# Performance work log

Measured on AMD Instinct MI355X. Metric: run time of the kernel, lower is better.

Reference implementation:

```python
import jax, jax.numpy as jnp
import numpy as np

N_NODES = 100000
N_EDGES = 1600000
F_IN = 128
H = 128
N_GRAPHS = 64
NEG_SLOPE = 0.2  # PyG GATConv default


def setup_inputs() -> dict:
    key = jax.random.key(0)
    ks = jax.random.split(key, 9)
    x = jax.random.normal(ks[0], (N_NODES, F_IN), dtype=jnp.float32)
    edge_index = jax.random.randint(ks[1], (2, N_EDGES), 0, N_NODES, dtype=jnp.int32)
    batch = jnp.sort(jax.random.randint(ks[2], (N_NODES,), 0, N_GRAPHS, dtype=jnp.int32))
    W = jax.random.normal(ks[3], (F_IN, H), dtype=jnp.float32) * 0.05
    att_src = jax.random.normal(ks[4], (H,), dtype=jnp.float32) * 0.05
    att_dst = jax.random.normal(ks[5], (H,), dtype=jnp.float32) * 0.05
    bias = jax.random.normal(ks[6], (H,), dtype=jnp.float32) * 0.05
    fin_w = jax.random.normal(ks[7], (H, 1), dtype=jnp.float32) * 0.05
    fin_b = jax.random.normal(ks[8], (1,), dtype=jnp.float32) * 0.05
    return {"x": x, "edge_index": edge_index, "batch": batch, "W": W,
            "att_src": att_src, "att_dst": att_dst, "bias": bias,
            "fin_w": fin_w, "fin_b": fin_b}


def reference(x, edge_index, batch, W, att_src, att_dst, bias, fin_w, fin_b):
    n = x.shape[0]
    # add self loops (add_self_loops=True)
    loop = jnp.arange(n, dtype=edge_index.dtype)
    src = jnp.concatenate([edge_index[0], loop])  # [E+N]
    dst = jnp.concatenate([edge_index[1], loop])  # [E+N]
    h = x @ W                                     # [N,H]
    a_s = h @ att_src                             # [N]
    a_d = h @ att_dst                             # [N]
    e = jax.nn.leaky_relu(a_s[src] + a_d[dst], NEG_SLOPE)  # [E+N]
    # segment softmax over destination neighborhoods
    e_max = jax.ops.segment_max(e, dst, num_segments=n)
    e_exp = jnp.exp(e - e_max[dst])
    denom = jax.ops.segment_sum(e_exp, dst, num_segments=n)
    alpha = e_exp / denom[dst]                    # [E+N]
    agg = jax.ops.segment_sum(alpha[:, None] * h[src], dst, num_segments=n)  # [N,H]
    gnn_out = jax.nn.silu(agg + bias)             # [N,H]
    # global mean pool per graph
    cnt = jax.ops.segment_sum(jnp.ones((n,), dtype=x.dtype), batch, num_segments=N_GRAPHS)
    pooled = jax.ops.segment_sum(gnn_out, batch, num_segments=N_GRAPHS)
    pooled = pooled / jnp.maximum(cnt, 1.0)[:, None]  # [B,H]
    return pooled @ fin_w + fin_b                 # [B,1]
```

## Files before the change

### kernel.cpp

```cpp
#include <hip/hip_runtime.h>

#define NND 100000
#define NE  1600000
#define ET  (NE + NND)
#define HD  128
#define NGR 64
#define NEG 0.2f

#define PEB   16384
#define PBLK  ((ET + PEB - 1) / PEB)
#define NBK   ((NND + 511) / 512)

__device__ __forceinline__ unsigned f2bf(float x) {
  unsigned u = __builtin_bit_cast(unsigned, x);
  return (u + 0x7fffu + ((u >> 16) & 1u)) >> 16;
}
__device__ __forceinline__ float bflo(unsigned u) { return __builtin_bit_cast(float, u << 16); }
__device__ __forceinline__ float bfhi(unsigned u) { return __builtin_bit_cast(float, u & 0xffff0000u); }

__global__ __launch_bounds__(512, 1) void k_gemm(const float* __restrict__ x,
                                                 const float* __restrict__ W,
                                                 const float* __restrict__ att_s,
                                                 const float* __restrict__ att_d,
                                                 unsigned* __restrict__ h_bf,
                                                 float* __restrict__ a_s,
                                                 float* __restrict__ a_d) {
  __shared__ float Wl[128 * 128];
  __shared__ float xT[128 * 128];
  const int t = threadIdx.x;
  const int rbase = blockIdx.x * 128;
#pragma unroll
  for (int i = 0; i < 8; ++i) {
    int idx = i * 512 + t;
    int k = idx >> 5, j = (idx & 31) * 4;
    *(float4*)&Wl[k * 128 + j] = *(const float4*)&W[k * 128 + j];
  }
#pragma unroll
  for (int i = 0; i < 8; ++i) {
    int idx = i * 512 + t;
    int rl = idx >> 5, kq = idx & 31;
    int r = rbase + rl;
    float4 v = (r < NND) ? *(const float4*)&x[(size_t)r * 128 + kq * 4]
                         : make_float4(0.f, 0.f, 0.f, 0.f);
    int col = rl ^ ((kq & 7) << 2);
    xT[(kq * 4 + 0) * 128 + col] = v.x;
    xT[(kq * 4 + 1) * 128 + col] = v.y;
    xT[(kq * 4 + 2) * 128 + col] = v.z;
    xT[(kq * 4 + 3) * 128 + col] = v.w;
  }
  __syncthreads();
  const int tc = t & 15, tr = t >> 4;
  float acc[4][8] = {};
#pragma unroll 4
  for (int k = 0; k < 128; ++k) {
    int ra = (4 * tr) ^ (((k >> 2) & 7) << 2);
    float4 xa = *(const float4*)&xT[k * 128 + ra];
    float4 wa = *(const float4*)&Wl[k * 128 + 4 * tc];
    float4 wb = *(const float4*)&Wl[k * 128 + 64 + 4 * tc];
    float xr[4] = {xa.x, xa.y, xa.z, xa.w};
    float wc[8] = {wa.x, wa.y, wa.z, wa.w, wb.x, wb.y, wb.z, wb.w};
#pragma unroll
    for (int i = 0; i < 4; ++i)
#pragma unroll
      for (int j = 0; j < 8; ++j) acc[i][j] = fmaf(xr[i], wc[j], acc[i][j]);
  }
  float asv[8], adv[8];
  {
    float4 a0 = *(const float4*)&att_s[4 * tc];
    float4 a1 = *(const float4*)&att_s[64 + 4 * tc];
    asv[0]=a0.x; asv[1]=a0.y; asv[2]=a0.z; asv[3]=a0.w;
    asv[4]=a1.x; asv[5]=a1.y; asv[6]=a1.z; asv[7]=a1.w;
    float4 b0 = *(const float4*)&att_d[4 * tc];
    float4 b1 = *(const float4*)&att_d[64 + 4 * tc];
    adv[0]=b0.x; adv[1]=b0.y; adv[2]=b0.z; adv[3]=b0.w;
    adv[4]=b1.x; adv[5]=b1.y; adv[6]=b1.z; adv[7]=b1.w;
  }
#pragma unroll
  for (int i = 0; i < 4; ++i) {
    int r = rbase + 4 * tr + i;
    float ps = 0.f, pd = 0.f;
#pragma unroll
    for (int j = 0; j < 8; ++j) {
      ps = fmaf(acc[i][j], asv[j], ps);
      pd = fmaf(acc[i][j], adv[j], pd);
    }
#pragma unroll
    for (int o = 1; o < 16; o <<= 1) {
      ps += __shfl_xor(ps, o);
      pd += __shfl_xor(pd, o);
    }
    if (r < NND) {
      if (tc == 0) { a_s[r] = ps; a_d[r] = pd; }
      unsigned p0 = f2bf(acc[i][0]) | (f2bf(acc[i][1]) << 16);
      unsigned p1 = f2bf(acc[i][2]) | (f2bf(acc[i][3]) << 16);
      unsigned p2 = f2bf(acc[i][4]) | (f2bf(acc[i][5]) << 16);
      unsigned p3 = f2bf(acc[i][6]) | (f2bf(acc[i][7]) << 16);
      *(uint2*)&h_bf[(size_t)r * 64 + 2 * tc] = make_uint2(p0, p1);
      *(uint2*)&h_bf[(size_t)r * 64 + 32 + 2 * tc] = make_uint2(p2, p3);
    }
  }
}

__global__ __launch_bounds__(1024) void k_hist(const int* __restrict__ ei,
                                               int* __restrict__ hist) {
  __shared__ int hcnt[256];
  const int t = threadIdx.x;
  if (t < 256) hcnt[t] = 0;
  __syncthreads();
  const int base = blockIdx.x * PEB;
#pragma unroll
  for (int i = 0; i < PEB / 1024; ++i) {
    int e = base + i * 1024 + t;
    if (e < ET) {
      int d = (e < NE) ? ei[NE + e] : (e - NE);
      atomicAdd(&hcnt[d >> 9], 1);
    }
  }
  __syncthreads();
  if (t < 256) hist[blockIdx.x * 256 + t] = hcnt[t];
}

__global__ __launch_bounds__(256) void k_hoff(int* __restrict__ hist,
                                              int* __restrict__ bkoff,
                                              int* __restrict__ bkcnt) {
  __shared__ int sm[2][256];
  const int t = threadIdx.x;
  int run = 0;
  for (int b = 0; b < PBLK; ++b) {
    int v = hist[b * 256 + t];
    hist[b * 256 + t] = run;
    run += v;
  }
  sm[0][t] = run;
  __syncthreads();
  int c = 0;
  for (int o = 1; o < 256; o <<= 1) {
    int val = sm[c][t];
    if (t >= o) val += sm[c][t - o];
    sm[c ^ 1][t] = val;
    c ^= 1;
    __syncthreads();
  }
  int bstart = sm[c][t] - run;
  bkoff[t] = bstart;
  bkcnt[t] = run;
  for (int b = 0; b < PBLK; ++b) hist[b * 256 + t] += bstart;
}

__global__ __launch_bounds__(1024) void k_part(const int* __restrict__ ei,
                                               const int* __restrict__ hist,
                                               uint2* __restrict__ part) {
  __shared__ int hcur[256];
  const int t = threadIdx.x;
  if (t < 256) hcur[t] = hist[blockIdx.x * 256 + t];
  __syncthreads();
  const int base = blockIdx.x * PEB;
#pragma unroll
  for (int i = 0; i < PEB / 1024; ++i) {
    int e = base + i * 1024 + t;
    if (e < ET) {
      int s, d;
      if (e < NE) { s = ei[e]; d = ei[NE + e]; } else { s = e - NE; d = s; }
      int pos = atomicAdd(&hcur[d >> 9], 1);
      part[pos] = make_uint2((unsigned)s, (unsigned)d);
    }
  }
}

__global__ __launch_bounds__(256) void k_bdeg(const uint2* __restrict__ part,
                                              const int* __restrict__ bkoff,
                                              const int* __restrict__ bkcnt,
                                              int* __restrict__ deg) {
  __shared__ int dcnt[512];
  const int t = threadIdx.x;
  const int b = blockIdx.x;
  dcnt[t] = 0; dcnt[t + 256] = 0;
  __syncthreads();
  const int lo = bkoff[b], n = bkcnt[b];
  for (int i = t; i < n; i += 256)
    atomicAdd(&dcnt[part[lo + i].y & 511], 1);
  __syncthreads();
#pragma unroll
  for (int j = t; j < 512; j += 256) {
    int node = b * 512 + j;
    if (node < NND) deg[node] = dcnt[j];
  }
}

__global__ __launch_bounds__(256) void k_scan1(const int* __restrict__ deg,
                                               int* __restrict__ off,
                                               int* __restrict__ bsum) {
  __shared__ int sm[2][256];
  int t = threadIdx.x;
  int i = blockIdx.x * 256 + t;
  int v = (i < NND) ? deg[i] : 0;
  sm[0][t] = v;
  __syncthreads();
  int c = 0;
  for (int o = 1; o < 256; o <<= 1) {
    int val = sm[c][t];
    if (t >= o) val += sm[c][t - o];
    sm[c ^ 1][t] = val;
    c ^= 1;
    __syncthreads();
  }
  int incl = sm[c][t];
  if (i < NND) off[i] = incl - v;
  if (t == 255) bsum[blockIdx.x] = incl;
}

__global__ __launch_bounds__(512) void k_scan2(int* __restrict__ bsum) {
  __shared__ int sm[2][512];
  const int NB = 391;
  int t = threadIdx.x;
  int v = (t < NB) ? bsum[t] : 0;
  sm[0][t] = v;
  __syncthreads();
  int c = 0;
  for (int o = 1; o < 512; o <<= 1) {
    int val = sm[c][t];
    if (t >= o) val += sm[c][t - o];
    sm[c ^ 1][t] = val;
    c ^= 1;
    __syncthreads();
  }
  if (t < NB) bsum[t] = sm[c][t] - v;
}

__global__ void k_scan3(const int* __restrict__ bsum, int* __restrict__ off) {
  int i = blockIdx.x * 256 + threadIdx.x;
  if (i < NND) off[i] += bsum[blockIdx.x];
}

__global__ __launch_bounds__(256) void k_bscat(const uint2* __restrict__ part,
                                               const int* __restrict__ bkoff,
                                               const int* __restrict__ bkcnt,
                                               const int* __restrict__ off,
                                               int* __restrict__ esrc) {
  __shared__ int curl[512];
  const int t = threadIdx.x;
  const int b = blockIdx.x;
#pragma unroll
  for (int j = t; j < 512; j += 256) {
    int node = b * 512 + j;
    curl[j] = (node < NND) ? off[node] : 0;
  }
  __syncthreads();
  const int lo = bkoff[b], n = bkcnt[b];
  for (int i = t; i < n; i += 256) {
    uint2 e = part[lo + i];
    int pos = atomicAdd(&curl[e.y & 511], 1);
    esrc[pos] = (int)e.x;
  }
}

__global__ __launch_bounds__(256) void k_agg(const int* __restrict__ off,
                                             const int* __restrict__ deg,
                                             const int* __restrict__ esrc,
                                             const float* __restrict__ a_s,
                                             const float* __restrict__ a_d,
                                             const unsigned* __restrict__ hb,
                                             const float* __restrict__ bias,
                                             unsigned* __restrict__ gnn) {
  int wid = (blockIdx.x * 256 + threadIdx.x) >> 6;
  int lane = threadIdx.x & 63;
  if (wid >= NND) return;
  const int grp = lane >> 4;
  const int lc  = lane & 15;
  int start = off[wid];
  int ne = deg[wid];
  float adn = a_d[wid];
  float acc[8] = {};
  float ssum = 0.f;
  for (int base = 0; base < ne; base += 64) {
    int i = base + lane;
    float ev = 0.f;
    int src = 0;
    if (i < ne) {
      src = esrc[start + i];
      float e = a_s[src] + adn;
      e = (e > 0.f) ? e : NEG * e;
      ev = __expf(e);
    }
    ssum += ev;
    int cnt = min(64, ne - base);
    for (int jj = 0; jj < cnt; jj += 4) {
      int idx = jj + grp;
      float p  = __shfl(ev, idx);
      int   sj = __shfl(src, idx);
      uint4 u = *((const uint4*)(hb + ((size_t)sj << 6)) + lc);
      acc[0] = fmaf(p, bflo(u.x), acc[0]);
      acc[1] = fmaf(p, bfhi(u.x), acc[1]);
      acc[2] = fmaf(p, bflo(u.y), acc[2]);
      acc[3] = fmaf(p, bfhi(u.y), acc[3]);
      acc[4] = fmaf(p, bflo(u.z), acc[4]);
      acc[5] = fmaf(p, bfhi(u.z), acc[5]);
      acc[6] = fmaf(p, bflo(u.w), acc[6]);
      acc[7] = fmaf(p, bfhi(u.w), acc[7]);
    }
  }
  for (int o = 32; o; o >>= 1) ssum += __shfl_xor(ssum, o);
#pragma unroll
  for (int r = 0; r < 8; ++r) {
    acc[r] += __shfl_xor(acc[r], 16);
    acc[r] += __shfl_xor(acc[r], 32);
  }
  if (grp == 0) {
    float inv = 1.f / ssum;
    float4 b0 = *(const float4*)&bias[lc * 8];
    float4 b1 = *(const float4*)&bias[lc * 8 + 4];
    float bb[8] = {b0.x, b0.y, b0.z, b0.w, b1.x, b1.y, b1.z, b1.w};
    float g[8];
#pragma unroll
    for (int r = 0; r < 8; ++r) {
      float v = acc[r] * inv + bb[r];
      g[r] = v / (1.f + __expf(-v));
    }
    unsigned w0 = f2bf(g[0]) | (f2bf(g[1]) << 16);
    unsigned w1 = f2bf(g[2]) | (f2bf(g[3]) << 16);
    unsigned w2 = f2bf(g[4]) | (f2bf(g[5]) << 16);
    unsigned w3 = f2bf(g[6]) | (f2bf(g[7]) << 16);
    *(uint4*)&gnn[(size_t)wid * 64 + lc * 4] = make_uint4(w0, w1, w2, w3);
  }
}

__global__ __launch_bounds__(256) void k_pool(const unsigned* __restrict__ gnn,
                                              const int* __restrict__ batch,
                                              float* __restrict__ pooled,
                                              float* __restrict__ cnt) {
  int t = threadIdx.x;
  int j2 = t & 63, strm = t >> 6;
  int base = blockIdx.x * 256;
  float ax = 0.f, ay = 0.f, c = 0.f;
  int curb = -1;
  for (int i = 0; i < 64; ++i) {
    int n = base + strm + i * 4;
    if (n >= NND) break;
    int b = batch[n];
    if (b != curb) {
      if (curb >= 0) {
        atomicAdd(&pooled[curb * HD + 2 * j2], ax);
        atomicAdd(&pooled[curb * HD + 2 * j2 + 1], ay);
        if (j2 == 0) atomicAdd(&cnt[curb], c);
      }
      curb = b; ax = 0.f; ay = 0.f; c = 0.f;
    }
    unsigned u = gnn[(size_t)n * 64 + j2];
    ax += bflo(u);
    ay += bfhi(u);
    c += 1.f;
  }
  if (curb >= 0) {
    atomicAdd(&pooled[curb * HD + 2 * j2], ax);
    atomicAdd(&pooled[curb * HD + 2 * j2 + 1], ay);
    if (j2 == 0) atomicAdd(&cnt[curb], c);
  }
}

__global__ void k_final(const float* __restrict__ pooled,
                        const float* __restrict__ cnt,
                        const float* __restrict__ fin_w,
                        const float* __restrict__ fin_b,
                        float* __restrict__ out) {
  int w = threadIdx.x >> 6, lane = threadIdx.x & 63;
  for (int g = w; g < NGR; g += 4) {
    float2 pv = *(const float2*)&pooled[g * HD + lane * 2];
    float2 fw = *(const float2*)&fin_w[lane * 2];
    float s = pv.x * fw.x + pv.y * fw.y;
    for (int o = 32; o; o >>= 1) s += __shfl_xor(s, o);
    if (lane == 0) out[g] = s / fmaxf(cnt[g], 1.f) + fin_b[0];
  }
}

extern "C" void kernel_launch(void* const* d_in, const int* in_sizes, int n_in,
                              void* d_out, int out_size, void* d_ws, size_t ws_size,
                              hipStream_t stream) {
  const float* x       = (const float*)d_in[0];
  const int*   ei      = (const int*)d_in[1];
  const int*   batch   = (const int*)d_in[2];
  const float* W       = (const float*)d_in[3];
  const float* att_src = (const float*)d_in[4];
  const float* att_dst = (const float*)d_in[5];
  const float* bias    = (const float*)d_in[6];
  const float* fin_w   = (const float*)d_in[7];
  const float* fin_b   = (const float*)d_in[8];
  float* out = (float*)d_out;

  float*    a_s  = (float*)d_ws;
  float*    a_d  = a_s + NND;
  unsigned* h_bf = (unsigned*)(a_d + NND);
  unsigned* gnn  = h_bf + (size_t)NND * 64;
  uint2*    part = (uint2*)(gnn + (size_t)NND * 64);
  int*      esrc = (int*)(part + ET);
  int*      off  = esrc + ET;
  int*      deg  = off + NND;
  int*      bsum = deg + NND;
  int*      hist = bsum + 512;
  int*      bkoff= hist + PBLK * 256;
  int*      bkcnt= bkoff + 256;
  float*  pooled = (float*)(bkcnt + 256);
  float*    cnt  = pooled + NGR * HD;

  hipMemsetAsync(pooled, 0, (size_t)(NGR * HD + NGR) * 4, stream);

  k_gemm <<<(NND + 127) / 128, 512, 0, stream>>>(x, W, att_src, att_dst, h_bf, a_s, a_d);
  k_hist <<<PBLK, 1024, 0, stream>>>(ei, hist);
  k_hoff <<<1, 256, 0, stream>>>(hist, bkoff, bkcnt);
  k_part <<<PBLK, 1024, 0, stream>>>(ei, hist, part);
  k_bdeg <<<NBK, 256, 0, stream>>>(part, bkoff, bkcnt, deg);
  k_scan1<<<391, 256, 0, stream>>>(deg, off, bsum);
  k_scan2<<<1, 512, 0, stream>>>(bsum);
  k_scan3<<<391, 256, 0, stream>>>(bsum, off);
  k_bscat<<<NBK, 256, 0, stream>>>(part, bkoff, bkcnt, off, esrc);
  k_agg  <<<25000, 256, 0, stream>>>(off, deg, esrc, a_s, a_d, h_bf, bias, gnn);
  k_pool <<<391, 256, 0, stream>>>(gnn, batch, pooled, cnt);
  k_final<<<1, 256, 0, stream>>>(pooled, cnt, fin_w, fin_b, out);
}
```

Measured before the change: 378.2 us.

## Replace FP32 LDS-tiled projection GEMM with bf16 MFMA kernel

Replaces the scalar-FMA shared-memory GEMM (x@W plus attention dot products) with a wave-level bf16 MFMA 16x16x32 kernel that reads x directly from global memory. W is pre-transposed to bf16 by a small new kernel, and the attention projections are computed from the MFMA accumulators using shuffle reductions. This is meant to cut the compute cost of the projection and to raise occupancy by dropping the 128KB LDS footprint. In exchange, x is now rounded to bf16 before the multiply, which lowers precision, and the output stores are narrower and scattered 4-byte writes.

```diff
diff --git a/kernel.cpp b/kernel.cpp
--- a/kernel.cpp
+++ b/kernel.cpp
@@ -11,6 +11,9 @@
 #define PBLK  ((ET + PEB - 1) / PEB)
 #define NBK   ((NND + 511) / 512)
 
+typedef __attribute__((ext_vector_type(8))) short short8;
+typedef __attribute__((ext_vector_type(4))) float f32x4;
+
 __device__ __forceinline__ unsigned f2bf(float x) {
   unsigned u = __builtin_bit_cast(unsigned, x);
   return (u + 0x7fffu + ((u >> 16) & 1u)) >> 16;
@@ -18,87 +21,80 @@
 __device__ __forceinline__ float bflo(unsigned u) { return __builtin_bit_cast(float, u << 16); }
 __device__ __forceinline__ float bfhi(unsigned u) { return __builtin_bit_cast(float, u & 0xffff0000u); }
 
-__global__ __launch_bounds__(512, 1) void k_gemm(const float* __restrict__ x,
-                                                 const float* __restrict__ W,
-                                                 const float* __restrict__ att_s,
-                                                 const float* __restrict__ att_d,
-                                                 unsigned* __restrict__ h_bf,
-                                                 float* __restrict__ a_s,
-                                                 float* __restrict__ a_d) {
-  __shared__ float Wl[128 * 128];
-  __shared__ float xT[128 * 128];
-  const int t = threadIdx.x;
-  const int rbase = blockIdx.x * 128;
-#pragma unroll
-  for (int i = 0; i < 8; ++i) {
-    int idx = i * 512 + t;
-    int k = idx >> 5, j = (idx & 31) * 4;
-    *(float4*)&Wl[k * 128 + j] = *(const float4*)&W[k * 128 + j];
-  }
-#pragma unroll
-  for (int i = 0; i < 8; ++i) {
-    int idx = i * 512 + t;
-    int rl = idx >> 5, kq = idx & 31;
-    int r = rbase + rl;
-    float4 v = (r < NND) ? *(const float4*)&x[(size_t)r * 128 + kq * 4]
-                         : make_float4(0.f, 0.f, 0.f, 0.f);
-    int col = rl ^ ((kq & 7) << 2);
-    xT[(kq * 4 + 0) * 128 + col] = v.x;
-    xT[(kq * 4 + 1) * 128 + col] = v.y;
-    xT[(kq * 4 + 2) * 128 + col] = v.z;
-    xT[(kq * 4 + 3) * 128 + col] = v.w;
-  }
-  __syncthreads();
-  const int tc = t & 15, tr = t >> 4;
-  float acc[4][8] = {};
-#pragma unroll 4
-  for (int k = 0; k < 128; ++k) {
-    int ra = (4 * tr) ^ (((k >> 2) & 7) << 2);
-    float4 xa = *(const float4*)&xT[k * 128 + ra];
-    float4 wa = *(const float4*)&Wl[k * 128 + 4 * tc];
-    float4 wb = *(const float4*)&Wl[k * 128 + 64 + 4 * tc];
-    float xr[4] = {xa.x, xa.y, xa.z, xa.w};
-    float wc[8] = {wa.x, wa.y, wa.z, wa.w, wb.x, wb.y, wb.z, wb.w};
-#pragma unroll
-    for (int i = 0; i < 4; ++i)
-#pragma unroll
-      for (int j = 0; j < 8; ++j) acc[i][j] = fmaf(xr[i], wc[j], acc[i][j]);
+__global__ void k_wt(const float* __restrict__ W, unsigned short* __restrict__ WT) {
+  int t = blockIdx.x * 256 + threadIdx.x;
+  int c = t >> 7, k = t & 127;
+  WT[t] = (unsigned short)f2bf(W[k * HD + c]);
+}
+
+__global__ __launch_bounds__(256) void k_gemm(const float* __restrict__ x,
+                                              const unsigned short* __restrict__ WT,
+                                              const float* __restrict__ att_s,
+                                              const float* __restrict__ att_d,
+                                              unsigned* __restrict__ h_bf,
+                                              float* __restrict__ a_s,
+                                              float* __restrict__ a_d) {
+  const int t = threadIdx.x;
+  const int wv = t >> 6, l = t & 63;
+  const int lr = l & 15, lk = l >> 4;
+  const int arow = blockIdx.x * 64 + wv * 16 + lr;
+  const bool av = arow < NND;
+  const float* xrow = x + (size_t)(av ? arow : 0) * HD;
+  f32x4 acc[8];
+#pragma unroll
+  for (int j = 0; j < 8; ++j) acc[j] = (f32x4){0.f, 0.f, 0.f, 0.f};
+#pragma unroll 1
+  for (int s = 0; s < 4; ++s) {
+    const int k0 = s * 32 + lk * 8;
+    float4 x0 = av ? *(const float4*)&xrow[k0]     : make_float4(0.f, 0.f, 0.f, 0.f);
+    float4 x1 = av ? *(const float4*)&xrow[k0 + 4] : make_float4(0.f, 0.f, 0.f, 0.f);
+    short8 af;
+    af[0] = (short)f2bf(x0.x); af[1] = (short)f2bf(x0.y);
+    af[2] = (short)f2bf(x0.z); af[3] = (short)f2bf(x0.w);
+    af[4] = (short)f2bf(x1.x); af[5] = (short)f2bf(x1.y);
+    af[6] = (short)f2bf(x1.z); af[7] = (short)f2bf(x1.w);
+#pragma unroll
+    for (int j = 0; j < 8; ++j) {
+      short8 bf8 = *(const short8*)&WT[(size_t)(j * 16 + lr) * HD + k0];
+      acc[j] = __builtin_amdgcn_mfma_f32_16x16x32_bf16(af, bf8, acc[j], 0, 0, 0);
+    }
   }
   float asv[8], adv[8];
-  {
-    float4 a0 = *(const float4*)&att_s[4 * tc];
-    float4 a1 = *(const float4*)&att_s[64 + 4 * tc];
-    asv[0]=a0.x; asv[1]=a0.y; asv[2]=a0.z; asv[3]=a0.w;
-    asv[4]=a1.x; asv[5]=a1.y; asv[6]=a1.z; asv[7]=a1.w;
-    float4 b0 = *(const float4*)&att_d[4 * tc];
-    float4 b1 = *(const float4*)&att_d[64 + 4 * tc];
-    adv[0]=b0.x; adv[1]=b0.y; adv[2]=b0.z; adv[3]=b0.w;
-    adv[4]=b1.x; adv[5]=b1.y; adv[6]=b1.z; adv[7]=b1.w;
-  }
-#pragma unroll
-  for (int i = 0; i < 4; ++i) {
-    int r = rbase + 4 * tr + i;
-    float ps = 0.f, pd = 0.f;
-#pragma unroll
-    for (int j = 0; j < 8; ++j) {
-      ps = fmaf(acc[i][j], asv[j], ps);
-      pd = fmaf(acc[i][j], adv[j], pd);
-    }
-#pragma unroll
-    for (int o = 1; o < 16; o <<= 1) {
-      ps += __shfl_xor(ps, o);
-      pd += __shfl_xor(pd, o);
-    }
-    if (r < NND) {
-      if (tc == 0) { a_s[r] = ps; a_d[r] = pd; }
-      unsigned p0 = f2bf(acc[i][0]) | (f2bf(acc[i][1]) << 16);
-      unsigned p1 = f2bf(acc[i][2]) | (f2bf(acc[i][3]) << 16);
-      unsigned p2 = f2bf(acc[i][4]) | (f2bf(acc[i][5]) << 16);
-      unsigned p3 = f2bf(acc[i][6]) | (f2bf(acc[i][7]) << 16);
-      *(uint2*)&h_bf[(size_t)r * 64 + 2 * tc] = make_uint2(p0, p1);
-      *(uint2*)&h_bf[(size_t)r * 64 + 32 + 2 * tc] = make_uint2(p2, p3);
-    }
-  }
+#pragma unroll
+  for (int j = 0; j < 8; ++j) { asv[j] = att_s[j * 16 + lr]; adv[j] = att_d[j * 16 + lr]; }
+  float pa[4] = {0.f, 0.f, 0.f, 0.f}, pd[4] = {0.f, 0.f, 0.f, 0.f};
+#pragma unroll
+  for (int j = 0; j < 8; ++j)
+#pragma unroll
+    for (int r = 0; r < 4; ++r) {
+      pa[r] = fmaf(acc[j][r], asv[j], pa[r]);
+      pd[r] = fmaf(acc[j][r], adv[j], pd[r]);
+    }
+#pragma unroll
+  for (int o = 1; o < 16; o <<= 1)
+#pragma unroll
+    for (int r = 0; r < 4; ++r) {
+      pa[r] += __shfl_xor(pa[r], o);
+      pd[r] += __shfl_xor(pd[r], o);
+    }
+  const int rbase = blockIdx.x * 64 + wv * 16 + lk * 4;
+#pragma unroll
+  for (int r = 0; r < 4; ++r) {
+    int row = rbase + r;
+    if (row < NND && lr == 0) { a_s[row] = pa[r]; a_d[row] = pd[r]; }
+  }
+#pragma unroll
+  for (int j = 0; j < 8; ++j)
+#pragma unroll
+    for (int r = 0; r < 4; ++r) {
+      float v = acc[j][r];
+      float vn = __shfl_xor(v, 1);
+      int row = rbase + r;
+      if ((lr & 1) == 0 && row < NND) {
+        unsigned w = f2bf(v) | (f2bf(vn) << 16);
+        h_bf[(size_t)row * 64 + ((j * 16 + lr) >> 1)] = w;
+      }
+    }
 }
 
 __global__ __launch_bounds__(1024) void k_hist(const int* __restrict__ ei,
@@ -400,10 +396,12 @@
   int*      bkcnt= bkoff + 256;
   float*  pooled = (float*)(bkcnt + 256);
   float*    cnt  = pooled + NGR * HD;
+  unsigned short* WT = (unsigned short*)(cnt + NGR);
 
   hipMemsetAsync(pooled, 0, (size_t)(NGR * HD + NGR) * 4, stream);
 
-  k_gemm <<<(NND + 127) / 128, 512, 0, stream>>>(x, W, att_src, att_dst, h_bf, a_s, a_d);
+  k_wt   <<<64, 256, 0, stream>>>(W, WT);
+  k_gemm <<<(NND + 63) / 64, 256, 0, stream>>>(x, WT, att_src, att_dst, h_bf, a_s, a_d);
   k_hist <<<PBLK, 1024, 0, stream>>>(ei, hist);
   k_hoff <<<1, 256, 0, stream>>>(hist, bkoff, bkcnt);
   k_part <<<PBLK, 1024, 0, stream>>>(ei, hist, part);
```

Result: faster. 348.2 us (-7.9%).
